# Kernel tuning notes

Hardware: AMD Instinct MI355X
Metric: run time of the kernel (lower is better)

The kernel has to match this reference:

```python
import jax, jax.numpy as jnp
import numpy as np

B, T, E = 32, 2048, 1024

def setup_inputs() -> dict:
    key = jax.random.key(0)
    k1, k2, k3 = jax.random.split(key, 3)
    enc = jax.random.normal(k1, (B, T, E), dtype=jnp.float32)
    ctx = jax.random.normal(k2, (B, E), dtype=jnp.float32)
    W = jax.random.normal(k3, (E, E), dtype=jnp.float32) * 0.05
    b = jnp.zeros((1, E), dtype=jnp.float32)
    return {"enc": enc, "ctx": ctx, "W": W, "b": b}

def reference(enc, ctx, W, b):
    # ht: (B, T, E) = tanh(enc @ W + b)
    ht = jnp.tanh(jnp.einsum('bte,ef->btf', enc, W) + b)
    # scores: (B, T) = batch dot of ctx against each timestep of ht
    scores = jnp.einsum('be,bte->bt', ctx, ht)
    at = jax.nn.softmax(scores, axis=-1)
    # weighted sum pooling over time -> (B, E)
    return jnp.einsum('bt,bte->be', at, ht)
```

## Files before the change

### kernel.cpp

```cpp
#include <hip/hip_runtime.h>
#include <hip/hip_bf16.h>
#include <math.h>

typedef unsigned short u16;
typedef unsigned int   u32;
typedef _Float16 f16x8 __attribute__((ext_vector_type(8)));
typedef float f32x4  __attribute__((ext_vector_type(4)));

#define Bb 32
#define Tt 2048
#define Ee 1024
#define Mm (Bb*Tt)

__device__ __forceinline__ float tanh_fast(float x) {
  float ax = fminf(fabsf(x), 15.0f);
  float e  = __expf(2.0f * ax);
  float t  = 1.0f - 2.0f / (e + 1.0f);
  return copysignf(t, x);
}

__device__ __forceinline__ u32 pack2h(float a, float b) {
  _Float16 ha = (_Float16)a, hb = (_Float16)b;
  return (u32)__builtin_bit_cast(u16, ha) | ((u32)__builtin_bit_cast(u16, hb) << 16);
}

__device__ __forceinline__ void glds16(const u16* g, u16* l) {
  __builtin_amdgcn_global_load_lds(
      (const __attribute__((address_space(1))) void*)g,
      (__attribute__((address_space(3))) void*)l, 16, 0, 0);
}

__global__ __launch_bounds__(256) void wt_convert(const float* __restrict__ W,
                                                  u16* __restrict__ Wt_hi,
                                                  u16* __restrict__ Wt_lo) {
  __shared__ float tile[32][33];
  int n0 = blockIdx.x * 32, k0 = blockIdx.y * 32;
  int tx = threadIdx.x, ty = threadIdx.y;
#pragma unroll
  for (int i = 0; i < 4; ++i)
    tile[ty + 8*i][tx] = W[(size_t)(k0 + ty + 8*i) * Ee + n0 + tx];
  __syncthreads();
#pragma unroll
  for (int i = 0; i < 4; ++i) {
    float v = tile[tx][ty + 8*i];
    _Float16 hi = (_Float16)v;
    float rem = v - (float)hi;
    _Float16 lo = (_Float16)rem;
    size_t idx = (size_t)(n0 + ty + 8*i) * Ee + k0 + tx;
    Wt_hi[idx] = __builtin_bit_cast(u16, hi);
    Wt_lo[idx] = __builtin_bit_cast(u16, lo);
  }
}

__global__ __launch_bounds__(256, 2) void gemm_tanh_score(
    const float* __restrict__ enc, const float* __restrict__ ctx,
    const float* __restrict__ bias,
    const u16* __restrict__ Wt_hi, const u16* __restrict__ Wt_lo,
    u16* __restrict__ ht, float* __restrict__ scores) {
  __shared__ __align__(16) u16 Ah [2*8192];
  __shared__ __align__(16) u16 BhS[2*4096];
  __shared__ __align__(16) u16 BlS[2*4096];

  int bx = blockIdx.x;
  int xcd = bx & 7, lb = bx >> 3;
  int nt = lb & 7, mtl = lb >> 3;
  int mt = xcd * 32 + mtl;
  int m0 = mt * 256, n0 = nt * 128;

  int tid = threadIdx.x;
  int w = tid >> 6, lane = tid & 63;
  int wm = (w & 1) * 128, wn = (w >> 1) * 64;
  int q = lane >> 4, c = lane & 15;
  int fch = (q ^ ((c >> 1) & 3)) * 8;

  f32x4 zero = {0.f, 0.f, 0.f, 0.f};
  f32x4 acc[8][4];
#pragma unroll
  for (int i = 0; i < 8; ++i)
#pragma unroll
    for (int j = 0; j < 4; ++j) acc[i][j] = zero;

  int arow = tid >> 3, ac8 = tid & 7;
  const float4* Abase = (const float4*)enc + ((size_t)(m0 + arow) * Ee >> 2) + ac8;
  int awbase = arow * 32 + (((ac8 >> 1) ^ ((arow >> 1) & 3)) << 3) + (ac8 & 1) * 4;

  int cidx0 = w * 2, cidx1 = w * 2 + 1;
  int r0 = cidx0 * 16 + (lane >> 2);
  int r1 = cidx1 * 16 + (lane >> 2);
  int lg0 = ((lane & 3) ^ ((r0 >> 1) & 3)) * 8;
  int lg1 = ((lane & 3) ^ ((r1 >> 1) & 3)) * 8;
  const u16* Bh0 = Wt_hi + (size_t)(n0 + r0) * Ee + lg0;
  const u16* Bh1 = Wt_hi + (size_t)(n0 + r1) * Ee + lg1;
  const u16* Bl0 = Wt_lo + (size_t)(n0 + r0) * Ee + lg0;
  const u16* Bl1 = Wt_lo + (size_t)(n0 + r1) * Ee + lg1;
  int bws0 = cidx0 * 512, bws1 = cidx1 * 512;

  {
    glds16(Bh0, &BhS[bws0]);
    glds16(Bh1, &BhS[bws1]);
    glds16(Bl0, &BlS[bws0]);
    glds16(Bl1, &BlS[bws1]);
    float4 av[8];
#pragma unroll
    for (int p = 0; p < 8; ++p) av[p] = Abase[(size_t)(32 * p) * (Ee / 4)];
#pragma unroll
    for (int p = 0; p < 8; ++p)
      *(uint2*)&Ah[awbase + 1024 * p] =
          make_uint2(pack2h(av[p].x, av[p].y), pack2h(av[p].z, av[p].w));
    __syncthreads();
  }

#pragma unroll 2
  for (int kt = 0; kt < 32; ++kt) {
    int curA = (kt & 1) * 8192, nxtA = 8192 - curA;
    int curB = (kt & 1) * 4096, nxtB = 4096 - curB;
    float4 av[8];
    if (kt < 31) {
#pragma unroll
      for (int p = 0; p < 8; ++p)
        av[p] = Abase[(size_t)(32 * p) * (Ee / 4) + (kt + 1) * 8];
      size_t ko = (size_t)(kt + 1) * 32;
      glds16(Bh0 + ko, &BhS[nxtB + bws0]);
      glds16(Bh1 + ko, &BhS[nxtB + bws1]);
      glds16(Bl0 + ko, &BlS[nxtB + bws0]);
      glds16(Bl1 + ko, &BlS[nxtB + bws1]);
    }

    f16x8 aF[8];
#pragma unroll
    for (int i = 0; i < 8; ++i)
      aF[i] = *(const f16x8*)&Ah[curA + (wm + i * 16 + c) * 32 + fch];

    __builtin_amdgcn_s_setprio(1);
#pragma unroll
    for (int j = 0; j < 4; ++j) {
      f16x8 bH = *(const f16x8*)&BhS[curB + (wn + j * 16 + c) * 32 + fch];
      f16x8 bL = *(const f16x8*)&BlS[curB + (wn + j * 16 + c) * 32 + fch];
#pragma unroll
      for (int i = 0; i < 8; ++i) {
        acc[i][j] = __builtin_amdgcn_mfma_f32_16x16x32_f16(aF[i], bH, acc[i][j], 0, 0, 0);
        acc[i][j] = __builtin_amdgcn_mfma_f32_16x16x32_f16(aF[i], bL, acc[i][j], 0, 0, 0);
      }
    }
    __builtin_amdgcn_s_setprio(0);

    if (kt < 31) {
#pragma unroll
      for (int p = 0; p < 8; ++p)
        *(uint2*)&Ah[nxtA + awbase + 1024 * p] =
            make_uint2(pack2h(av[p].x, av[p].y), pack2h(av[p].z, av[p].w));
    }
    __syncthreads();
  }

  int bidx = m0 >> 11;
  float ctxv[4], biasv[4];
#pragma unroll
  for (int j = 0; j < 4; ++j) {
    int col = n0 + wn + j * 16 + c;
    ctxv[j]  = ctx[bidx * Ee + col];
    biasv[j] = bias[col];
  }
#pragma unroll
  for (int i = 0; i < 8; ++i) {
#pragma unroll
    for (int r = 0; r < 4; ++r) {
      int rowG = m0 + wm + i * 16 + q * 4 + r;
      u16* hrow = ht + (size_t)rowG * Ee + n0 + wn + c;
      float s = 0.f;
#pragma unroll
      for (int j = 0; j < 4; ++j) {
        float h = tanh_fast(acc[i][j][r] + biasv[j]);
        __hip_bfloat16 hb = __float2bfloat16(h);
        hrow[j * 16] = *(u16*)&hb;
        s += h * ctxv[j];
      }
      s += __shfl_xor(s, 1); s += __shfl_xor(s, 2);
      s += __shfl_xor(s, 4); s += __shfl_xor(s, 8);
      if (c == 0) atomicAdd(&scores[rowG], s);
    }
  }
}

__global__ __launch_bounds__(256) void softmax_t(const float* __restrict__ scores,
                                                 float* __restrict__ at) {
  __shared__ float red[256];
  int b = blockIdx.x, tid = threadIdx.x;
  float v[8];
  float mx = -3.0e38f;
#pragma unroll
  for (int i = 0; i < 8; ++i) {
    v[i] = scores[b * Tt + i * 256 + tid];
    mx = fmaxf(mx, v[i]);
  }
  red[tid] = mx; __syncthreads();
  for (int s = 128; s > 0; s >>= 1) {
    if (tid < s) red[tid] = fmaxf(red[tid], red[tid + s]);
    __syncthreads();
  }
  mx = red[0]; __syncthreads();
  float sum = 0.f;
#pragma unroll
  for (int i = 0; i < 8; ++i) { v[i] = __expf(v[i] - mx); sum += v[i]; }
  red[tid] = sum; __syncthreads();
  for (int s = 128; s > 0; s >>= 1) {
    if (tid < s) red[tid] += red[tid + s];
    __syncthreads();
  }
  float inv = 1.0f / red[0];
#pragma unroll
  for (int i = 0; i < 8; ++i) at[b * Tt + i * 256 + tid] = v[i] * inv;
}

__global__ __launch_bounds__(256) void weighted_sum(const u16* __restrict__ ht,
                                                    const float* __restrict__ at,
                                                    float* __restrict__ part) {
  __shared__ float ats[64];
  int bx = blockIdx.x;
  int b = bx >> 5, tc = bx & 31;
  int tid = threadIdx.x;
  if (tid < 64) ats[tid] = at[b * Tt + tc * 64 + tid];
  __syncthreads();
  int e0 = tid * 4;
  const u16* base = ht + (size_t)(b * Tt + tc * 64) * Ee + e0;
  float s0 = 0.f, s1 = 0.f, s2 = 0.f, s3 = 0.f;
#pragma unroll 4
  for (int t = 0; t < 64; ++t) {
    float a = ats[t];
    uint2 u = *(const uint2*)(base + (size_t)t * Ee);
    s0 += a * __uint_as_float(u.x << 16);
    s1 += a * __uint_as_float(u.x & 0xffff0000u);
    s2 += a * __uint_as_float(u.y << 16);
    s3 += a * __uint_as_float(u.y & 0xffff0000u);
  }
  float4 out4 = make_float4(s0, s1, s2, s3);
  *(float4*)(part + ((size_t)(b * 32 + tc) * Ee + e0)) = out4;
}

__global__ __launch_bounds__(256) void reduce_part(const float* __restrict__ part,
                                                   float* __restrict__ out) {
  int b = blockIdx.x, tid = threadIdx.x;
  float4 s = make_float4(0.f, 0.f, 0.f, 0.f);
#pragma unroll
  for (int tc = 0; tc < 32; ++tc) {
    float4 p = ((const float4*)(part + (size_t)(b * 32 + tc) * Ee))[tid];
    s.x += p.x; s.y += p.y; s.z += p.z; s.w += p.w;
  }
  ((float4*)(out + (size_t)b * Ee))[tid] = s;
}

extern "C" void kernel_launch(void* const* d_in, const int* in_sizes, int n_in,
                              void* d_out, int out_size, void* d_ws, size_t ws_size,
                              hipStream_t stream) {
  const float* enc  = (const float*)d_in[0];
  const float* ctx  = (const float*)d_in[1];
  const float* W    = (const float*)d_in[2];
  const float* bias = (const float*)d_in[3];
  float* out = (float*)d_out;

  char* ws = (char*)d_ws;
  u16* Wt_hi = (u16*)(ws);
  u16* Wt_lo = (u16*)(ws + (size_t)2 * 1024 * 1024);
  u16* ht    = (u16*)(ws + (size_t)4 * 1024 * 1024);
  float* scores = (float*)(ws + (size_t)4 * 1024 * 1024 + (size_t)Mm * Ee * 2);
  float* at     = scores + Mm;
  float* part   = (float*)ws;

  hipMemsetAsync(scores, 0, (size_t)Mm * sizeof(float), stream);

  wt_convert<<<dim3(32, 32), dim3(32, 8), 0, stream>>>(W, Wt_hi, Wt_lo);
  gemm_tanh_score<<<dim3(2048), dim3(256), 0, stream>>>(enc, ctx, bias, Wt_hi, Wt_lo, ht, scores);
  softmax_t<<<dim3(32), dim3(256), 0, stream>>>(scores, at);
  weighted_sum<<<dim3(1024), dim3(256), 0, stream>>>(ht, at, part);
  reduce_part<<<dim3(32), dim3(256), 0, stream>>>(part, out);
}
```

Baseline: 652.0 us.

## Triple-buffer B tiles with depth-2 prefetch and phase-split MFMA schedule

Turns the shared-memory pipeline for the W hi/lo tiles into a three-deep ring buffer that prefetches two K-steps ahead. The A tile drops to a single buffer, and the loop is split into four MFMA phases per K-step. Global loads of A are staggered between phases, and explicit barriers, waitcnts and sched_barriers control the interleave. The aim is to hide global-to-LDS latency behind the MFMA work, at the cost of many more barriers per iteration and tighter hand-managed synchronisation.

```diff
diff --git a/kernel.cpp b/kernel.cpp
--- a/kernel.cpp
+++ b/kernel.cpp
@@ -57,9 +57,9 @@
     const float* __restrict__ bias,
     const u16* __restrict__ Wt_hi, const u16* __restrict__ Wt_lo,
     u16* __restrict__ ht, float* __restrict__ scores) {
-  __shared__ __align__(16) u16 Ah [2*8192];
-  __shared__ __align__(16) u16 BhS[2*4096];
-  __shared__ __align__(16) u16 BlS[2*4096];
+  __shared__ __align__(16) u16 Ah [8192];
+  __shared__ __align__(16) u16 BhS[3*4096];
+  __shared__ __align__(16) u16 BlS[3*4096];
 
   int bx = blockIdx.x;
   int xcd = bx & 7, lb = bx >> 3;
@@ -96,10 +96,14 @@
   int bws0 = cidx0 * 512, bws1 = cidx1 * 512;
 
   {
-    glds16(Bh0, &BhS[bws0]);
-    glds16(Bh1, &BhS[bws1]);
-    glds16(Bl0, &BlS[bws0]);
-    glds16(Bl1, &BlS[bws1]);
+    glds16(Bh0, &BhS[0 + bws0]);
+    glds16(Bh1, &BhS[0 + bws1]);
+    glds16(Bl0, &BlS[0 + bws0]);
+    glds16(Bl1, &BlS[0 + bws1]);
+    glds16(Bh0 + 32, &BhS[4096 + bws0]);
+    glds16(Bh1 + 32, &BhS[4096 + bws1]);
+    glds16(Bl0 + 32, &BlS[4096 + bws0]);
+    glds16(Bl1 + 32, &BlS[4096 + bws1]);
     float4 av[8];
 #pragma unroll
     for (int p = 0; p < 8; ++p) av[p] = Abase[(size_t)(32 * p) * (Ee / 4)];
@@ -110,48 +114,79 @@
     __syncthreads();
   }
 
-#pragma unroll 2
+  int b0 = 0, b1 = 4096, b2 = 8192;
+
+#define MFMA_PHASE(J, BH, BL)                                                  \
+  {                                                                            \
+    __builtin_amdgcn_s_barrier();                                              \
+    asm volatile("s_waitcnt lgkmcnt(0)" ::: "memory");                         \
+    __builtin_amdgcn_sched_barrier(0);                                         \
+    __builtin_amdgcn_s_setprio(1);                                             \
+    _Pragma("unroll")                                                          \
+    for (int i = 0; i < 8; ++i) {                                              \
+      acc[i][J] = __builtin_amdgcn_mfma_f32_16x16x32_f16(aF[i], BH, acc[i][J], 0, 0, 0); \
+      acc[i][J] = __builtin_amdgcn_mfma_f32_16x16x32_f16(aF[i], BL, acc[i][J], 0, 0, 0); \
+    }                                                                          \
+    __builtin_amdgcn_s_setprio(0);                                             \
+    __builtin_amdgcn_s_barrier();                                              \
+  }
+
+#pragma unroll 1
   for (int kt = 0; kt < 32; ++kt) {
-    int curA = (kt & 1) * 8192, nxtA = 8192 - curA;
-    int curB = (kt & 1) * 4096, nxtB = 4096 - curB;
     float4 av[8];
     if (kt < 31) {
 #pragma unroll
+      for (int p = 0; p < 4; ++p)
+        av[p] = Abase[(size_t)(32 * p) * (Ee / 4) + (size_t)(kt + 1) * 8];
+    }
+    f16x8 aF[8];
+#pragma unroll
+    for (int i = 0; i < 8; ++i)
+      aF[i] = *(const f16x8*)&Ah[(wm + i * 16 + c) * 32 + fch];
+    {
+      f16x8 bH = *(const f16x8*)&BhS[b0 + (wn + 0 * 16 + c) * 32 + fch];
+      f16x8 bL = *(const f16x8*)&BlS[b0 + (wn + 0 * 16 + c) * 32 + fch];
+      MFMA_PHASE(0, bH, bL)
+    }
+    if (kt < 31) {
+#pragma unroll
+      for (int p = 4; p < 8; ++p)
+        av[p] = Abase[(size_t)(32 * p) * (Ee / 4) + (size_t)(kt + 1) * 8];
+    }
+    {
+      f16x8 bH = *(const f16x8*)&BhS[b0 + (wn + 1 * 16 + c) * 32 + fch];
+      f16x8 bL = *(const f16x8*)&BlS[b0 + (wn + 1 * 16 + c) * 32 + fch];
+      MFMA_PHASE(1, bH, bL)
+    }
+    {
+      f16x8 bH = *(const f16x8*)&BhS[b0 + (wn + 2 * 16 + c) * 32 + fch];
+      f16x8 bL = *(const f16x8*)&BlS[b0 + (wn + 2 * 16 + c) * 32 + fch];
+      MFMA_PHASE(2, bH, bL)
+    }
+    if (kt < 30) {
+      size_t ko = (size_t)(kt + 2) * 32;
+      glds16(Bh0 + ko, &BhS[b2 + bws0]);
+      glds16(Bh1 + ko, &BhS[b2 + bws1]);
+      glds16(Bl0 + ko, &BlS[b2 + bws0]);
+      glds16(Bl1 + ko, &BlS[b2 + bws1]);
+    }
+    {
+      f16x8 bH = *(const f16x8*)&BhS[b0 + (wn + 3 * 16 + c) * 32 + fch];
+      f16x8 bL = *(const f16x8*)&BlS[b0 + (wn + 3 * 16 + c) * 32 + fch];
+      MFMA_PHASE(3, bH, bL)
+    }
+    if (kt < 31) {
+      asm volatile("s_waitcnt vmcnt(4)" ::: "memory");
+#pragma unroll
       for (int p = 0; p < 8; ++p)
-        av[p] = Abase[(size_t)(32 * p) * (Ee / 4) + (kt + 1) * 8];
-      size_t ko = (size_t)(kt + 1) * 32;
-      glds16(Bh0 + ko, &BhS[nxtB + bws0]);
-      glds16(Bh1 + ko, &BhS[nxtB + bws1]);
-      glds16(Bl0 + ko, &BlS[nxtB + bws0]);
-      glds16(Bl1 + ko, &BlS[nxtB + bws1]);
-    }
-
-    f16x8 aF[8];
-#pragma unroll
-    for (int i = 0; i < 8; ++i)
-      aF[i] = *(const f16x8*)&Ah[curA + (wm + i * 16 + c) * 32 + fch];
-
-    __builtin_amdgcn_s_setprio(1);
-#pragma unroll
-    for (int j = 0; j < 4; ++j) {
-      f16x8 bH = *(const f16x8*)&BhS[curB + (wn + j * 16 + c) * 32 + fch];
-      f16x8 bL = *(const f16x8*)&BlS[curB + (wn + j * 16 + c) * 32 + fch];
-#pragma unroll
-      for (int i = 0; i < 8; ++i) {
-        acc[i][j] = __builtin_amdgcn_mfma_f32_16x16x32_f16(aF[i], bH, acc[i][j], 0, 0, 0);
-        acc[i][j] = __builtin_amdgcn_mfma_f32_16x16x32_f16(aF[i], bL, acc[i][j], 0, 0, 0);
-      }
-    }
-    __builtin_amdgcn_s_setprio(0);
-
-    if (kt < 31) {
-#pragma unroll
-      for (int p = 0; p < 8; ++p)
-        *(uint2*)&Ah[nxtA + awbase + 1024 * p] =
+        *(uint2*)&Ah[awbase + 1024 * p] =
             make_uint2(pack2h(av[p].x, av[p].y), pack2h(av[p].z, av[p].w));
     }
-    __syncthreads();
-  }
+    asm volatile("s_waitcnt lgkmcnt(0)" ::: "memory");
+    __builtin_amdgcn_s_barrier();
+    int tmp = b0; b0 = b1; b1 = b2; b2 = tmp;
+  }
+#undef MFMA_PHASE
 
   int bidx = m0 >> 11;
   float ctxv[4], biasv[4];
```

New measurement: 802.5 us. 1.23x slower.

## Pre-convert enc to fp16 and stream A tiles via direct-to-LDS triple buffering

Applied to the files above, without the earlier changes.

Adds a separate pass that converts enc from fp32 to fp16 in workspace. The GEMM then loads A with global_load_lds into a triple-buffered LDS ring, prefetching two k-steps ahead with explicit waitcnt and barriers, instead of loading fp32 into registers, converting, and storing to LDS. This is meant to halve A traffic in the GEMM and take the conversion off its critical path. In exchange it adds a full extra read of enc plus an fp16 write and re-read (about 128MB extra fp16 traffic), and falls back to the old fp32 path when the workspace is too small.

```diff
diff --git a/kernel.cpp b/kernel.cpp
--- a/kernel.cpp
+++ b/kernel.cpp
@@ -28,6 +28,20 @@
   __builtin_amdgcn_global_load_lds(
       (const __attribute__((address_space(1))) void*)g,
       (__attribute__((address_space(3))) void*)l, 16, 0, 0);
+}
+
+__global__ __launch_bounds__(256) void enc_convert(const float* __restrict__ enc,
+                                                   u16* __restrict__ enc16) {
+  size_t i = ((size_t)blockIdx.x * 256 + threadIdx.x) * 8;
+  size_t stride = (size_t)gridDim.x * 256 * 8;
+  size_t total = (size_t)Mm * Ee;
+  for (; i < total; i += stride) {
+    float4 f0 = *(const float4*)(enc + i);
+    float4 f1 = *(const float4*)(enc + i + 4);
+    uint4 o = make_uint4(pack2h(f0.x, f0.y), pack2h(f0.z, f0.w),
+                         pack2h(f1.x, f1.y), pack2h(f1.z, f1.w));
+    *(uint4*)(enc16 + i) = o;
+  }
 }
 
 __global__ __launch_bounds__(256) void wt_convert(const float* __restrict__ W,
@@ -52,12 +66,12 @@
   }
 }
 
-__global__ __launch_bounds__(256, 2) void gemm_tanh_score(
-    const float* __restrict__ enc, const float* __restrict__ ctx,
+__global__ __launch_bounds__(256, 2) void gemm_tanh_score16(
+    const u16* __restrict__ enc16, const float* __restrict__ ctx,
     const float* __restrict__ bias,
     const u16* __restrict__ Wt_hi, const u16* __restrict__ Wt_lo,
     u16* __restrict__ ht, float* __restrict__ scores) {
-  __shared__ __align__(16) u16 Ah [2*8192];
+  __shared__ __align__(16) u16 Ah [3*8192];
   __shared__ __align__(16) u16 BhS[2*4096];
   __shared__ __align__(16) u16 BlS[2*4096];
 
@@ -80,9 +94,14 @@
 #pragma unroll
     for (int j = 0; j < 4; ++j) acc[i][j] = zero;
 
-  int arow = tid >> 3, ac8 = tid & 7;
-  const float4* Abase = (const float4*)enc + ((size_t)(m0 + arow) * Ee >> 2) + ac8;
-  int awbase = arow * 32 + (((ac8 >> 1) ^ ((arow >> 1) & 3)) << 3) + (ac8 & 1) * 4;
+  int lgA = (((lane & 3) ^ ((lane >> 3) & 3))) * 8;
+  int arw = (lane >> 2);
+  const u16* A0 = enc16 + (size_t)(m0 + w * 64 +  0 + arw) * Ee + lgA;
+  const u16* A1 = enc16 + (size_t)(m0 + w * 64 + 16 + arw) * Ee + lgA;
+  const u16* A2 = enc16 + (size_t)(m0 + w * 64 + 32 + arw) * Ee + lgA;
+  const u16* A3 = enc16 + (size_t)(m0 + w * 64 + 48 + arw) * Ee + lgA;
+  int aws0 = (w * 4 + 0) * 512, aws1 = (w * 4 + 1) * 512;
+  int aws2 = (w * 4 + 2) * 512, aws3 = (w * 4 + 3) * 512;
 
   int cidx0 = w * 2, cidx1 = w * 2 + 1;
   int r0 = cidx0 * 16 + (lane >> 2);
@@ -96,17 +115,152 @@
   int bws0 = cidx0 * 512, bws1 = cidx1 * 512;
 
   {
+    glds16(A0, &Ah[0 + aws0]); glds16(A1, &Ah[0 + aws1]);
+    glds16(A2, &Ah[0 + aws2]); glds16(A3, &Ah[0 + aws3]);
+    glds16(Bh0, &BhS[bws0]);   glds16(Bh1, &BhS[bws1]);
+    glds16(Bl0, &BlS[bws0]);   glds16(Bl1, &BlS[bws1]);
+    glds16(A0 + 32, &Ah[8192 + aws0]); glds16(A1 + 32, &Ah[8192 + aws1]);
+    glds16(A2 + 32, &Ah[8192 + aws2]); glds16(A3 + 32, &Ah[8192 + aws3]);
+    asm volatile("s_waitcnt vmcnt(4)" ::: "memory");
+    __builtin_amdgcn_s_barrier();
+    __builtin_amdgcn_sched_barrier(0);
+  }
+
+  int a0 = 0, a1 = 8192, a2 = 16384;
+
+#pragma unroll 1
+  for (int kt = 0; kt < 32; ++kt) {
+    int curB = (kt & 1) * 4096, nxtB = 4096 - curB;
+    if (kt < 31) {
+      size_t ko = (size_t)(kt + 1) * 32;
+      glds16(Bh0 + ko, &BhS[nxtB + bws0]);
+      glds16(Bh1 + ko, &BhS[nxtB + bws1]);
+      glds16(Bl0 + ko, &BlS[nxtB + bws0]);
+      glds16(Bl1 + ko, &BlS[nxtB + bws1]);
+    }
+    if (kt < 30) {
+      size_t ka = (size_t)(kt + 2) * 32;
+      glds16(A0 + ka, &Ah[a2 + aws0]);
+      glds16(A1 + ka, &Ah[a2 + aws1]);
+      glds16(A2 + ka, &Ah[a2 + aws2]);
+      glds16(A3 + ka, &Ah[a2 + aws3]);
+    }
+
+    f16x8 aF[8];
+#pragma unroll
+    for (int i = 0; i < 8; ++i)
+      aF[i] = *(const f16x8*)&Ah[a0 + (wm + i * 16 + c) * 32 + fch];
+
+    __builtin_amdgcn_s_setprio(1);
+#pragma unroll
+    for (int j = 0; j < 4; ++j) {
+      f16x8 bH = *(const f16x8*)&BhS[curB + (wn + j * 16 + c) * 32 + fch];
+      f16x8 bL = *(const f16x8*)&BlS[curB + (wn + j * 16 + c) * 32 + fch];
+#pragma unroll
+      for (int i = 0; i < 8; ++i)
+        acc[i][j] = __builtin_amdgcn_mfma_f32_16x16x32_f16(aF[i], bH, acc[i][j], 0, 0, 0);
+#pragma unroll
+      for (int i = 0; i < 8; ++i)
+        acc[i][j] = __builtin_amdgcn_mfma_f32_16x16x32_f16(aF[i], bL, acc[i][j], 0, 0, 0);
+    }
+    __builtin_amdgcn_s_setprio(0);
+
+    if (kt < 30) asm volatile("s_waitcnt vmcnt(4)" ::: "memory");
+    else         asm volatile("s_waitcnt vmcnt(0)" ::: "memory");
+    __builtin_amdgcn_s_barrier();
+    __builtin_amdgcn_sched_barrier(0);
+    int tmp = a0; a0 = a1; a1 = a2; a2 = tmp;
+  }
+
+  int bidx = m0 >> 11;
+  float ctxv[4], biasv[4];
+#pragma unroll
+  for (int j = 0; j < 4; ++j) {
+    int col = n0 + wn + j * 16 + c;
+    ctxv[j]  = ctx[bidx * Ee + col];
+    biasv[j] = bias[col];
+  }
+#pragma unroll
+  for (int i = 0; i < 8; ++i) {
+#pragma unroll
+    for (int r = 0; r < 4; ++r) {
+      int rowG = m0 + wm + i * 16 + q * 4 + r;
+      u16* hrow = ht + (size_t)rowG * Ee + n0 + wn + c;
+      float s = 0.f;
+#pragma unroll
+      for (int j = 0; j < 4; ++j) {
+        float h = tanh_fast(acc[i][j][r] + biasv[j]);
+        __hip_bfloat16 hb = __float2bfloat16(h);
+        hrow[j * 16] = *(u16*)&hb;
+        s += h * ctxv[j];
+      }
+      s += __shfl_xor(s, 1); s += __shfl_xor(s, 2);
+      s += __shfl_xor(s, 4); s += __shfl_xor(s, 8);
+      if (c == 0) atomicAdd(&scores[rowG], s);
+    }
+  }
+}
+
+__global__ __launch_bounds__(256, 2) void gemm_tanh_score_f32(
+    const float* __restrict__ enc, const float* __restrict__ ctx,
+    const float* __restrict__ bias,
+    const u16* __restrict__ Wt_hi, const u16* __restrict__ Wt_lo,
+    u16* __restrict__ ht, float* __restrict__ scores) {
+  __shared__ __align__(16) u16 Ah [2*8192];
+  __shared__ __align__(16) u16 BhS[2*4096];
+  __shared__ __align__(16) u16 BlS[2*4096];
+
+  int bx = blockIdx.x;
+  int xcd = bx & 7, lb = bx >> 3;
+  int nt = lb & 7, mtl = lb >> 3;
+  int mt = xcd * 32 + mtl;
+  int m0 = mt * 256, n0 = nt * 128;
+
+  int tid = threadIdx.x;
+  int w = tid >> 6, lane = tid & 63;
+  int wm = (w & 1) * 128, wn = (w >> 1) * 64;
+  int q = lane >> 4, c = lane & 15;
+  int fch = (q ^ ((c >> 1) & 3)) * 8;
+
+  f32x4 zero = {0.f, 0.f, 0.f, 0.f};
+  f32x4 acc[8][4];
+#pragma unroll
+  for (int i = 0; i < 8; ++i)
+#pragma unroll
+    for (int j = 0; j < 4; ++j) acc[i][j] = zero;
+
+  int arow = tid >> 3, ac8 = tid & 7;
+  const float4* Abase = (const float4*)enc + ((size_t)(m0 + arow) * Ee >> 2) + ac8;
+  int awbase = arow * 32 + (((ac8 >> 1) ^ ((arow >> 1) & 3)) << 3) + (ac8 & 1) * 4;
+
+  int cidx0 = w * 2, cidx1 = w * 2 + 1;
+  int r0 = cidx0 * 16 + (lane >> 2);
+  int r1 = cidx1 * 16 + (lane >> 2);
+  int lg0 = ((lane & 3) ^ ((r0 >> 1) & 3)) * 8;
+  int lg1 = ((lane & 3) ^ ((r1 >> 1) & 3)) * 8;
+  const u16* Bh0 = Wt_hi + (size_t)(n0 + r0) * Ee + lg0;
+  const u16* Bh1 = Wt_hi + (size_t)(n0 + r1) * Ee + lg1;
+  const u16* Bl0 = Wt_lo + (size_t)(n0 + r0) * Ee + lg0;
+  const u16* Bl1 = Wt_lo + (size_t)(n0 + r1) * Ee + lg1;
+  int bws0 = cidx0 * 512, bws1 = cidx1 * 512;
+
+  {
     glds16(Bh0, &BhS[bws0]);
     glds16(Bh1, &BhS[bws1]);
     glds16(Bl0, &BlS[bws0]);
     glds16(Bl1, &BlS[bws1]);
-    float4 av[8];
-#pragma unroll
-    for (int p = 0; p < 8; ++p) av[p] = Abase[(size_t)(32 * p) * (Ee / 4)];
-#pragma unroll
-    for (int p = 0; p < 8; ++p)
-      *(uint2*)&Ah[awbase + 1024 * p] =
-          make_uint2(pack2h(av[p].x, av[p].y), pack2h(av[p].z, av[p].w));
+    float4 f0 = Abase[0], f1 = Abase[(size_t)32 * (Ee/4)],
+           f2 = Abase[(size_t)64 * (Ee/4)], f3 = Abase[(size_t)96 * (Ee/4)];
+    float4 f4 = Abase[(size_t)128 * (Ee/4)], f5 = Abase[(size_t)160 * (Ee/4)],
+           f6 = Abase[(size_t)192 * (Ee/4)], f7 = Abase[(size_t)224 * (Ee/4)];
+    *(uint2*)&Ah[awbase + 0]    = make_uint2(pack2h(f0.x,f0.y), pack2h(f0.z,f0.w));
+    *(uint2*)&Ah[awbase + 1024] = make_uint2(pack2h(f1.x,f1.y), pack2h(f1.z,f1.w));
+    *(uint2*)&Ah[awbase + 2048] = make_uint2(pack2h(f2.x,f2.y), pack2h(f2.z,f2.w));
+    *(uint2*)&Ah[awbase + 3072] = make_uint2(pack2h(f3.x,f3.y), pack2h(f3.z,f3.w));
+    *(uint2*)&Ah[awbase + 4096] = make_uint2(pack2h(f4.x,f4.y), pack2h(f4.z,f4.w));
+    *(uint2*)&Ah[awbase + 5120] = make_uint2(pack2h(f5.x,f5.y), pack2h(f5.z,f5.w));
+    *(uint2*)&Ah[awbase + 6144] = make_uint2(pack2h(f6.x,f6.y), pack2h(f6.z,f6.w));
+    *(uint2*)&Ah[awbase + 7168] = make_uint2(pack2h(f7.x,f7.y), pack2h(f7.z,f7.w));
     __syncthreads();
   }
 
@@ -118,7 +272,7 @@
     if (kt < 31) {
 #pragma unroll
       for (int p = 0; p < 8; ++p)
-        av[p] = Abase[(size_t)(32 * p) * (Ee / 4) + (kt + 1) * 8];
+        av[p] = Abase[(size_t)(32 * p) * (Ee / 4) + (size_t)(kt + 1) * 8];
       size_t ko = (size_t)(kt + 1) * 32;
       glds16(Bh0 + ko, &BhS[nxtB + bws0]);
       glds16(Bh1 + ko, &BhS[nxtB + bws1]);
@@ -264,12 +418,24 @@
   u16* ht    = (u16*)(ws + (size_t)4 * 1024 * 1024);
   float* scores = (float*)(ws + (size_t)4 * 1024 * 1024 + (size_t)Mm * Ee * 2);
   float* at     = scores + Mm;
-  float* part   = (float*)ws;
+  u16* enc16 = (u16*)(ws + (size_t)4 * 1024 * 1024 + (size_t)Mm * Ee * 2
+                         + (size_t)Mm * 8);
+  float* part = (float*)ws;
+
+  size_t need = (size_t)4 * 1024 * 1024 + (size_t)Mm * Ee * 2 + (size_t)Mm * 8
+              + (size_t)Mm * Ee * 2;
 
   hipMemsetAsync(scores, 0, (size_t)Mm * sizeof(float), stream);
-
   wt_convert<<<dim3(32, 32), dim3(32, 8), 0, stream>>>(W, Wt_hi, Wt_lo);
-  gemm_tanh_score<<<dim3(2048), dim3(256), 0, stream>>>(enc, ctx, bias, Wt_hi, Wt_lo, ht, scores);
+
+  if (ws_size >= need) {
+    enc_convert<<<dim3(8192), dim3(256), 0, stream>>>(enc, enc16);
+    gemm_tanh_score16<<<dim3(2048), dim3(256), 0, stream>>>(enc16, ctx, bias,
+                                                            Wt_hi, Wt_lo, ht, scores);
+  } else {
+    gemm_tanh_score_f32<<<dim3(2048), dim3(256), 0, stream>>>(enc, ctx, bias,
+                                                              Wt_hi, Wt_lo, ht, scores);
+  }
   softmax_t<<<dim3(32), dim3(256), 0, stream>>>(scores, at);
   weighted_sum<<<dim3(1024), dim3(256), 0, stream>>>(ht, at, part);
   reduce_part<<<dim3(32), dim3(256), 0, stream>>>(part, out);
```

Result: slower. 691.1 us (+6.0%).
